# Kernel tuning notes

Measured on AMD Instinct MI355X. Metric: run time of the kernel, lower is better.

Reference implementation:

```python
import jax, jax.numpy as jnp
import numpy as np

B, C, H, W = 16, 3, 384, 1280
EPS = 1e-7


def setup_inputs() -> dict:
    key = jax.random.key(0)
    k1, k2, k3, k4 = jax.random.split(key, 4)
    source_image = jax.random.normal(k1, (B, C, H, W), jnp.float32)
    depth_map = jax.random.uniform(k2, (B, 1, H, W), jnp.float32, minval=0.1, maxval=80.0)
    pose = 0.05 * jax.random.normal(k3, (B, 6), jnp.float32)
    # realistic KITTI-style pinhole intrinsics, per-batch mild perturbation
    base = jnp.array([[0.58 * W, 0.0, 0.5 * W],
                      [0.0, 1.92 * H, 0.5 * H],
                      [0.0, 0.0, 1.0]], jnp.float32)
    noise = 1.0 + 0.01 * jax.random.normal(k4, (B, 3, 3), jnp.float32)
    intrinsic = base[None] * noise  # zero entries stay zero -> invertible
    return {"source_image": source_image, "depth_map": depth_map,
            "pose": pose, "intrinsic": intrinsic}


def rot_from_axisangle(aa):
    # aa: [B,3] -> [B,3,3] (Rodrigues)
    theta = jnp.linalg.norm(aa, axis=-1, keepdims=True)  # [B,1]
    axis = aa / (theta + EPS)
    c = jnp.cos(theta)
    s = jnp.sin(theta)
    t = 1.0 - c
    x, y, z = axis[:, 0:1], axis[:, 1:2], axis[:, 2:3]
    row0 = jnp.concatenate([t * x * x + c, t * x * y - s * z, t * z * x + s * y], axis=1)
    row1 = jnp.concatenate([t * x * y + s * z, t * y * y + c, t * y * z - s * x], axis=1)
    row2 = jnp.concatenate([t * z * x - s * y, t * y * z + s * x, t * z * z + c], axis=1)
    return jnp.stack([row0, row1, row2], axis=1)  # [B,3,3]


def bilinear_grid_sample(img, gx, gy):
    # img: [B,C,H,W]; gx,gy: [B,H,W] in [-1,1]; align_corners=True, padding zeros
    Bc, Cc, Hc, Wc = img.shape
    x = (gx + 1.0) * 0.5 * (Wc - 1)
    y = (gy + 1.0) * 0.5 * (Hc - 1)
    x0 = jnp.floor(x)
    y0 = jnp.floor(y)
    x1 = x0 + 1.0
    y1 = y0 + 1.0
    wx1 = x - x0
    wx0 = 1.0 - wx1
    wy1 = y - y0
    wy0 = 1.0 - wy1
    imgf = img.reshape(Bc, Cc, Hc * Wc)

    def gather(xi, yi):
        inb = ((xi >= 0) & (xi <= Wc - 1) & (yi >= 0) & (yi <= Hc - 1)).astype(img.dtype)
        xc = jnp.clip(xi, 0, Wc - 1).astype(jnp.int32)
        yc = jnp.clip(yi, 0, Hc - 1).astype(jnp.int32)
        idx = (yc * Wc + xc).reshape(Bc, 1, -1)
        vals = jnp.take_along_axis(imgf, jnp.broadcast_to(idx, (Bc, Cc, idx.shape[-1])), axis=2)
        return vals.reshape(Bc, Cc, Hc, Wc) * inb[:, None]

    out = (gather(x0, y0) * (wx0 * wy0)[:, None]
           + gather(x1, y0) * (wx1 * wy0)[:, None]
           + gather(x0, y1) * (wx0 * wy1)[:, None]
           + gather(x1, y1) * (wx1 * wy1)[:, None])
    return out


def reference(source_image, depth_map, pose, intrinsic):
    Bb, _, Hh, Ww = depth_map.shape
    # pixel grid, homogeneous [H,W,3] = (x, y, 1)
    ys, xs = jnp.meshgrid(jnp.arange(Hh, dtype=depth_map.dtype),
                          jnp.arange(Ww, dtype=depth_map.dtype), indexing='ij')
    pix = jnp.stack([xs, ys, jnp.ones_like(xs)], axis=-1)  # [H,W,3]
    # backproject: K^{-1} @ pix * depth
    inv_K = jnp.linalg.inv(intrinsic)  # [B,3,3]
    cam = jnp.einsum('bij,hwj->bhwi', inv_K, pix)  # [B,H,W,3]
    frustum = cam * jnp.transpose(depth_map, (0, 2, 3, 1))  # [B,H,W,3]
    # rigid transform
    R = rot_from_axisangle(pose[:, :3])  # [B,3,3]
    t = pose[:, 3:]  # [B,3]
    points = jnp.einsum('bij,bhwj->bhwi', R, frustum) + t[:, None, None, :]
    # project with K
    coord = jnp.einsum('bij,bhwj->bhwi', intrinsic, points)  # [B,H,W,3]
    z = coord[..., 2] + EPS
    px = coord[..., 0] / z
    py = coord[..., 1] / z
    gx = px / (Ww - 1) * 2.0 - 1.0
    gy = py / (Hh - 1) * 2.0 - 1.0
    return bilinear_grid_sample(source_image, gx, gy)
```

## Files before the change

kernel.cpp:

```cpp
#include <hip/hip_runtime.h>

#define B_ 16
#define C_ 3
#define H_ 384
#define W_ 1280
#define HW_ (H_*W_)
#define EPS_ 1e-7f

__device__ __forceinline__ void mat3mul(const float* A, const float* Bm, float* C) {
  #pragma unroll
  for (int i = 0; i < 3; i++)
    #pragma unroll
    for (int j = 0; j < 3; j++)
      C[i*3+j] = A[i*3+0]*Bm[0*3+j] + A[i*3+1]*Bm[1*3+j] + A[i*3+2]*Bm[2*3+j];
}

__device__ void compute_MT(const float* __restrict__ pose,
                           const float* __restrict__ intr,
                           int b, float* M, float* T)
{
  float K[9];
  #pragma unroll
  for (int i = 0; i < 9; i++) K[i] = intr[b*9 + i];
  float aa0 = pose[b*6 + 0];
  float aa1 = pose[b*6 + 1];
  float aa2 = pose[b*6 + 2];
  float t0  = pose[b*6 + 3];
  float t1  = pose[b*6 + 4];
  float t2  = pose[b*6 + 5];

  float theta = sqrtf(aa0*aa0 + aa1*aa1 + aa2*aa2);
  float invn  = 1.0f / (theta + EPS_);
  float x = aa0*invn, y = aa1*invn, z = aa2*invn;
  float c = cosf(theta), s = sinf(theta), t = 1.0f - c;
  float R[9] = {
    t*x*x + c,   t*x*y - s*z, t*z*x + s*y,
    t*x*y + s*z, t*y*y + c,   t*y*z - s*x,
    t*z*x - s*y, t*y*z + s*x, t*z*z + c
  };

  float a = K[0], bb = K[1], cc = K[2];
  float d = K[3], e  = K[4], f  = K[5];
  float g = K[6], h  = K[7], ii = K[8];
  float A0 = e*ii - f*h;
  float A1 = f*g  - d*ii;
  float A2 = d*h  - e*g;
  float det = a*A0 + bb*A1 + cc*A2;
  float id  = 1.0f / det;
  float iK[9] = {
    A0*id, (cc*h - bb*ii)*id, (bb*f - cc*e)*id,
    A1*id, (a*ii - cc*g)*id,  (cc*d - a*f)*id,
    A2*id, (bb*g - a*h)*id,   (a*e  - bb*d)*id
  };

  float KR[9];
  mat3mul(K, R, KR);
  mat3mul(KR, iK, M);
  T[0] = K[0]*t0 + K[1]*t1 + K[2]*t2;
  T[1] = K[3]*t0 + K[4]*t1 + K[5]*t2;
  T[2] = K[6]*t0 + K[7]*t1 + K[8]*t2;
}

__global__ void param_kernel(const float* __restrict__ pose,
                             const float* __restrict__ intr,
                             float* __restrict__ params)
{
  int b = threadIdx.x;
  if (b < B_) {
    float M[9], T[3];
    compute_MT(pose, intr, b, M, T);
    #pragma unroll
    for (int i = 0; i < 9; i++) params[b*12 + i] = M[i];
    #pragma unroll
    for (int i = 0; i < 3; i++) params[b*12 + 9 + i] = T[i];
  }
}

__global__ __launch_bounds__(256) void warp_kernel(
    const float* __restrict__ src,
    const float* __restrict__ depth,
    const float* __restrict__ params,
    const float* __restrict__ pose,
    const float* __restrict__ intr,
    float* __restrict__ out,
    int use_params)
{
  __shared__ float sp[12];
  int b = blockIdx.y;
  if (threadIdx.x == 0) {
    if (use_params) {
      #pragma unroll
      for (int i = 0; i < 12; i++) sp[i] = params[b*12 + i];
    } else {
      float M[9], T[3];
      compute_MT(pose, intr, b, M, T);
      #pragma unroll
      for (int i = 0; i < 9; i++) sp[i] = M[i];
      #pragma unroll
      for (int i = 0; i < 3; i++) sp[9 + i] = T[i];
    }
  }
  __syncthreads();
  float m00 = sp[0], m01 = sp[1], m02 = sp[2];
  float m10 = sp[3], m11 = sp[4], m12 = sp[5];
  float m20 = sp[6], m21 = sp[7], m22 = sp[8];
  float T0  = sp[9], T1  = sp[10], T2 = sp[11];

  int p = blockIdx.x * 256 + threadIdx.x;
  int j = p % W_;
  int i = p / W_;

  float d = depth[(size_t)b * HW_ + p];
  float xf = (float)j, yf = (float)i;

  float cx = (m00*xf + m01*yf + m02)*d + T0;
  float cy = (m10*xf + m11*yf + m12)*d + T1;
  float cz = (m20*xf + m21*yf + m22)*d + T2;
  float zz = cz + EPS_;
  float px = cx / zz;
  float py = cy / zz;

  float x0f = floorf(px), y0f = floorf(py);
  float x1f = x0f + 1.0f, y1f = y0f + 1.0f;
  float wx1 = px - x0f, wx0 = 1.0f - wx1;
  float wy1 = py - y0f, wy0 = 1.0f - wy1;

  float mx0 = (x0f >= 0.0f && x0f <= (float)(W_-1)) ? 1.0f : 0.0f;
  float mx1 = (x1f >= 0.0f && x1f <= (float)(W_-1)) ? 1.0f : 0.0f;
  float my0 = (y0f >= 0.0f && y0f <= (float)(H_-1)) ? 1.0f : 0.0f;
  float my1 = (y1f >= 0.0f && y1f <= (float)(H_-1)) ? 1.0f : 0.0f;

  int xc0 = (int)fminf(fmaxf(x0f, 0.0f), (float)(W_-1));
  int xc1 = (int)fminf(fmaxf(x1f, 0.0f), (float)(W_-1));
  int yc0 = (int)fminf(fmaxf(y0f, 0.0f), (float)(H_-1));
  int yc1 = (int)fminf(fmaxf(y1f, 0.0f), (float)(H_-1));

  int i00 = yc0*W_ + xc0;
  int i01 = yc0*W_ + xc1;
  int i10 = yc1*W_ + xc0;
  int i11 = yc1*W_ + xc1;

  float w00 = wx0*wy0*mx0*my0;
  float w01 = wx1*wy0*mx1*my0;
  float w10 = wx0*wy1*mx0*my1;
  float w11 = wx1*wy1*mx1*my1;

  size_t sb = (size_t)b * C_ * HW_;
  #pragma unroll
  for (int ch = 0; ch < C_; ch++) {
    const float* sc = src + sb + (size_t)ch * HW_;
    float v = sc[i00] * w00
            + sc[i01] * w01
            + sc[i10] * w10
            + sc[i11] * w11;
    out[sb + (size_t)ch * HW_ + p] = v;
  }
}

extern "C" void kernel_launch(void* const* d_in, const int* in_sizes, int n_in,
                              void* d_out, int out_size, void* d_ws, size_t ws_size,
                              hipStream_t stream) {
  const float* src   = (const float*)d_in[0];
  const float* depth = (const float*)d_in[1];
  const float* pose  = (const float*)d_in[2];
  const float* intr  = (const float*)d_in[3];
  float* out = (float*)d_out;

  int use_params = (d_ws != nullptr && ws_size >= (size_t)(B_*12*sizeof(float)))
                   ? 1 : 0;
  float* params = (float*)d_ws;

  if (use_params) {
    param_kernel<<<1, 64, 0, stream>>>(pose, intr, params);
  }
  dim3 grid(HW_ / 256, B_);
  warp_kernel<<<grid, 256, 0, stream>>>(src, depth, params, pose, intr, out,
                                        use_params);
}
```

Baseline: 256.5 us.

## Fuse param setup into warp kernel, process 8 rows per block, nontemporal IO

Drops the separate parameter kernel, so each block computes its own transform matrix. Each block now handles 8 image rows for a 256-pixel column strip in a 3D grid, which amortises the per-block setup and syncthreads and hoists the x-dependent terms. The per-pixel divisions become one reciprocal, and depth loads and output stores use nontemporal hints to avoid polluting the cache that serves the gathers. The trade-off is 8x fewer blocks, each doing serial work over its rows, and redundant matrix computation in every block.

Result: no change. 259.2 us (+1.0%).

```diff
diff --git a/kernel.cpp b/kernel.cpp
--- a/kernel.cpp
+++ b/kernel.cpp
@@ -6,6 +6,7 @@
 #define W_ 1280
 #define HW_ (H_*W_)
 #define EPS_ 1e-7f
+#define ROWS_ 8
 
 __device__ __forceinline__ void mat3mul(const float* A, const float* Bm, float* C) {
   #pragma unroll
@@ -22,12 +23,8 @@
   float K[9];
   #pragma unroll
   for (int i = 0; i < 9; i++) K[i] = intr[b*9 + i];
-  float aa0 = pose[b*6 + 0];
-  float aa1 = pose[b*6 + 1];
-  float aa2 = pose[b*6 + 2];
-  float t0  = pose[b*6 + 3];
-  float t1  = pose[b*6 + 4];
-  float t2  = pose[b*6 + 5];
+  float aa0 = pose[b*6 + 0], aa1 = pose[b*6 + 1], aa2 = pose[b*6 + 2];
+  float t0  = pose[b*6 + 3], t1  = pose[b*6 + 4], t2  = pose[b*6 + 5];
 
   float theta = sqrtf(aa0*aa0 + aa1*aa1 + aa2*aa2);
   float invn  = 1.0f / (theta + EPS_);
@@ -42,11 +39,8 @@
   float a = K[0], bb = K[1], cc = K[2];
   float d = K[3], e  = K[4], f  = K[5];
   float g = K[6], h  = K[7], ii = K[8];
-  float A0 = e*ii - f*h;
-  float A1 = f*g  - d*ii;
-  float A2 = d*h  - e*g;
-  float det = a*A0 + bb*A1 + cc*A2;
-  float id  = 1.0f / det;
+  float A0 = e*ii - f*h, A1 = f*g - d*ii, A2 = d*h - e*g;
+  float id = 1.0f / (a*A0 + bb*A1 + cc*A2);
   float iK[9] = {
     A0*id, (cc*h - bb*ii)*id, (bb*f - cc*e)*id,
     A1*id, (a*ii - cc*g)*id,  (cc*d - a*f)*id,
@@ -61,44 +55,22 @@
   T[2] = K[6]*t0 + K[7]*t1 + K[8]*t2;
 }
 
-__global__ void param_kernel(const float* __restrict__ pose,
-                             const float* __restrict__ intr,
-                             float* __restrict__ params)
+__global__ __launch_bounds__(256) void warp_kernel(
+    const float* __restrict__ src,
+    const float* __restrict__ depth,
+    const float* __restrict__ pose,
+    const float* __restrict__ intr,
+    float* __restrict__ out)
 {
-  int b = threadIdx.x;
-  if (b < B_) {
+  __shared__ float sp[12];
+  int b = blockIdx.z;
+  if (threadIdx.x == 0) {
     float M[9], T[3];
     compute_MT(pose, intr, b, M, T);
     #pragma unroll
-    for (int i = 0; i < 9; i++) params[b*12 + i] = M[i];
+    for (int i = 0; i < 9; i++) sp[i] = M[i];
     #pragma unroll
-    for (int i = 0; i < 3; i++) params[b*12 + 9 + i] = T[i];
-  }
-}
-
-__global__ __launch_bounds__(256) void warp_kernel(
-    const float* __restrict__ src,
-    const float* __restrict__ depth,
-    const float* __restrict__ params,
-    const float* __restrict__ pose,
-    const float* __restrict__ intr,
-    float* __restrict__ out,
-    int use_params)
-{
-  __shared__ float sp[12];
-  int b = blockIdx.y;
-  if (threadIdx.x == 0) {
-    if (use_params) {
-      #pragma unroll
-      for (int i = 0; i < 12; i++) sp[i] = params[b*12 + i];
-    } else {
-      float M[9], T[3];
-      compute_MT(pose, intr, b, M, T);
-      #pragma unroll
-      for (int i = 0; i < 9; i++) sp[i] = M[i];
-      #pragma unroll
-      for (int i = 0; i < 3; i++) sp[9 + i] = T[i];
-    }
+    for (int i = 0; i < 3; i++) sp[9 + i] = T[i];
   }
   __syncthreads();
   float m00 = sp[0], m01 = sp[1], m02 = sp[2];
@@ -106,54 +78,66 @@
   float m20 = sp[6], m21 = sp[7], m22 = sp[8];
   float T0  = sp[9], T1  = sp[10], T2 = sp[11];
 
-  int p = blockIdx.x * 256 + threadIdx.x;
-  int j = p % W_;
-  int i = p / W_;
+  int x    = blockIdx.x * 256 + threadIdx.x;
+  int row0 = blockIdx.y * ROWS_;
+  float xf = (float)x;
 
-  float d = depth[(size_t)b * HW_ + p];
-  float xf = (float)j, yf = (float)i;
-
-  float cx = (m00*xf + m01*yf + m02)*d + T0;
-  float cy = (m10*xf + m11*yf + m12)*d + T1;
-  float cz = (m20*xf + m21*yf + m22)*d + T2;
-  float zz = cz + EPS_;
-  float px = cx / zz;
-  float py = cy / zz;
-
-  float x0f = floorf(px), y0f = floorf(py);
-  float x1f = x0f + 1.0f, y1f = y0f + 1.0f;
-  float wx1 = px - x0f, wx0 = 1.0f - wx1;
-  float wy1 = py - y0f, wy0 = 1.0f - wy1;
-
-  float mx0 = (x0f >= 0.0f && x0f <= (float)(W_-1)) ? 1.0f : 0.0f;
-  float mx1 = (x1f >= 0.0f && x1f <= (float)(W_-1)) ? 1.0f : 0.0f;
-  float my0 = (y0f >= 0.0f && y0f <= (float)(H_-1)) ? 1.0f : 0.0f;
-  float my1 = (y1f >= 0.0f && y1f <= (float)(H_-1)) ? 1.0f : 0.0f;
-
-  int xc0 = (int)fminf(fmaxf(x0f, 0.0f), (float)(W_-1));
-  int xc1 = (int)fminf(fmaxf(x1f, 0.0f), (float)(W_-1));
-  int yc0 = (int)fminf(fmaxf(y0f, 0.0f), (float)(H_-1));
-  int yc1 = (int)fminf(fmaxf(y1f, 0.0f), (float)(H_-1));
-
-  int i00 = yc0*W_ + xc0;
-  int i01 = yc0*W_ + xc1;
-  int i10 = yc1*W_ + xc0;
-  int i11 = yc1*W_ + xc1;
-
-  float w00 = wx0*wy0*mx0*my0;
-  float w01 = wx1*wy0*mx1*my0;
-  float w10 = wx0*wy1*mx0*my1;
-  float w11 = wx1*wy1*mx1*my1;
+  float ax = m00*xf + m02;
+  float bx = m10*xf + m12;
+  float cxk = m20*xf + m22;
 
   size_t sb = (size_t)b * C_ * HW_;
-  #pragma unroll
-  for (int ch = 0; ch < C_; ch++) {
-    const float* sc = src + sb + (size_t)ch * HW_;
-    float v = sc[i00] * w00
-            + sc[i01] * w01
-            + sc[i10] * w10
-            + sc[i11] * w11;
-    out[sb + (size_t)ch * HW_ + p] = v;
+  const float* s0 = src + sb;
+  const float* s1 = s0 + HW_;
+  const float* s2 = s1 + HW_;
+
+  for (int r = 0; r < ROWS_; r++) {
+    int i = row0 + r;
+    float yf = (float)i;
+    size_t pix = (size_t)b * HW_ + (size_t)i * W_ + x;
+
+    float d = __builtin_nontemporal_load(&depth[pix]);
+
+    float cx = (m01*yf + ax)*d + T0;
+    float cy = (m11*yf + bx)*d + T1;
+    float cz = (m21*yf + cxk)*d + T2;
+    float zz = cz + EPS_;
+    float inv = 1.0f / zz;
+    float px = cx * inv;
+    float py = cy * inv;
+
+    float x0f = floorf(px), y0f = floorf(py);
+    float x1f = x0f + 1.0f, y1f = y0f + 1.0f;
+    float wx1 = px - x0f, wx0 = 1.0f - wx1;
+    float wy1 = py - y0f, wy0 = 1.0f - wy1;
+
+    float mx0 = (x0f >= 0.0f && x0f <= (float)(W_-1)) ? 1.0f : 0.0f;
+    float mx1 = (x1f >= 0.0f && x1f <= (float)(W_-1)) ? 1.0f : 0.0f;
+    float my0 = (y0f >= 0.0f && y0f <= (float)(H_-1)) ? 1.0f : 0.0f;
+    float my1 = (y1f >= 0.0f && y1f <= (float)(H_-1)) ? 1.0f : 0.0f;
+
+    int xc0 = (int)fminf(fmaxf(x0f, 0.0f), (float)(W_-1));
+    int xc1 = (int)fminf(fmaxf(x1f, 0.0f), (float)(W_-1));
+    int yc0 = (int)fminf(fmaxf(y0f, 0.0f), (float)(H_-1));
+    int yc1 = (int)fminf(fmaxf(y1f, 0.0f), (float)(H_-1));
+
+    int i00 = yc0*W_ + xc0;
+    int i01 = yc0*W_ + xc1;
+    int i10 = yc1*W_ + xc0;
+    int i11 = yc1*W_ + xc1;
+
+    float w00 = wx0*wy0*mx0*my0;
+    float w01 = wx1*wy0*mx1*my0;
+    float w10 = wx0*wy1*mx0*my1;
+    float w11 = wx1*wy1*mx1*my1;
+
+    size_t op = (size_t)i * W_ + x;
+    float v0 = s0[i00]*w00 + s0[i01]*w01 + s0[i10]*w10 + s0[i11]*w11;
+    float v1 = s1[i00]*w00 + s1[i01]*w01 + s1[i10]*w10 + s1[i11]*w11;
+    float v2 = s2[i00]*w00 + s2[i01]*w01 + s2[i10]*w10 + s2[i11]*w11;
+    __builtin_nontemporal_store(v0, &out[sb + op]);
+    __builtin_nontemporal_store(v1, &out[sb + HW_ + op]);
+    __builtin_nontemporal_store(v2, &out[sb + 2*(size_t)HW_ + op]);
   }
 }
 
@@ -166,14 +150,6 @@
   const float* intr  = (const float*)d_in[3];
   float* out = (float*)d_out;
 
-  int use_params = (d_ws != nullptr && ws_size >= (size_t)(B_*12*sizeof(float)))
-                   ? 1 : 0;
-  float* params = (float*)d_ws;
-
-  if (use_params) {
-    param_kernel<<<1, 64, 0, stream>>>(pose, intr, params);
-  }
-  dim3 grid(HW_ / 256, B_);
-  warp_kernel<<<grid, 256, 0, stream>>>(src, depth, params, pose, intr, out,
-                                        use_params);
+  dim3 grid(W_ / 256, H_ / ROWS_, B_);
+  warp_kernel<<<grid, 256, 0, stream>>>(src, depth, pose, intr, out);
 }
```
